# Kernel optimization log

Hardware: AMD Instinct MI355X
Metric: run time of the kernel (lower is better)

Reference implementation:

```python
import jax, jax.numpy as jnp
import numpy as np

N_NODES = 100000
N_EDGES = 1600000
F_IN = 128
F_OUT = 128


def setup_inputs() -> dict:
    key = jax.random.key(0)
    k1, k2, k3 = jax.random.split(key, 3)
    x = jax.random.normal(k1, (N_NODES, F_IN), dtype=jnp.float32)
    edge_index = jax.random.randint(k2, (2, N_EDGES), 0, N_NODES, dtype=jnp.int64)
    # glorot-ish init for GCNConv weight
    W = jax.random.normal(k3, (F_IN, F_OUT), dtype=jnp.float32) * (1.0 / np.sqrt(F_IN))
    b = jnp.zeros((F_OUT,), dtype=jnp.float32)
    return {"x": x, "edge_index": edge_index, "W": W, "b": b}


def gcn_conv(x, edge_index, W, b, num_nodes):
    # 1) linear transform
    h = x @ W  # [N, F_OUT]
    # 2) add self loops
    loop = jnp.arange(num_nodes, dtype=edge_index.dtype)
    src = jnp.concatenate([edge_index[0], loop])  # [E+N]
    dst = jnp.concatenate([edge_index[1], loop])  # [E+N]
    # 3) symmetric normalization: deg computed at targets (incl. self loops)
    ones = jnp.ones(src.shape[0], dtype=h.dtype)
    deg = jax.ops.segment_sum(ones, dst, num_segments=num_nodes)  # [N]
    dinv = jnp.where(deg > 0, jax.lax.rsqrt(deg), 0.0)
    norm = dinv[src] * dinv[dst]  # [E+N]
    # 4) message = norm * h[src]; scatter-add to dst
    msg = h[src] * norm[:, None]  # [E+N, F_OUT] (dominant memory traffic)
    out = jax.ops.segment_sum(msg, dst, num_segments=num_nodes)  # [N, F_OUT]
    return out + b


def reference(x, edge_index, W, b):
    out = gcn_conv(x, edge_index, W, b, N_NODES)
    return jax.nn.relu(out)
```

## Files before the change

### kernel.cpp

```cpp
#include <hip/hip_runtime.h>

#define F 128
#define CH 4096
#define BSH 9
#define BMSK ((1u << BSH) - 1u)

typedef __bf16 bf16x8 __attribute__((ext_vector_type(8)));
typedef float f32x4 __attribute__((ext_vector_type(4)));

__device__ inline uint32_t bfbits(float f) {
  uint32_t x = __float_as_uint(f);
  return (x + 0x7fffu + ((x >> 16) & 1u)) >> 16;
}
__device__ inline float blo(uint32_t u) { return __uint_as_float(u << 16); }
__device__ inline float bhi(uint32_t u) { return __uint_as_float(u & 0xffff0000u); }

__global__ __launch_bounds__(256) void k_gemm(const float* __restrict__ x,
                                              const float* __restrict__ W,
                                              const float* __restrict__ dinv,
                                              uint32_t* __restrict__ hB, int N) {
  __shared__ uint4 wb[2048];
  const int t = threadIdx.x;

#pragma unroll
  for (int p = 0; p < 8; ++p) {
    const int s = p * 256 + t;
    const int l = s & 63, nc = (s >> 6) & 7, kc = s >> 9;
    const int kbase = kc * 32 + ((l >> 4) << 3);
    const int col = nc * 16 + (l & 15);
    uint32_t q[4];
#pragma unroll
    for (int ii = 0; ii < 4; ++ii) {
      const uint32_t lo2 = bfbits(W[(size_t)(kbase + 2 * ii) * F + col]);
      const uint32_t hi2 = bfbits(W[(size_t)(kbase + 2 * ii + 1) * F + col]);
      q[ii] = lo2 | (hi2 << 16);
    }
    wb[s] = make_uint4(q[0], q[1], q[2], q[3]);
  }
  __syncthreads();

  const int w = t >> 6, l = t & 63;
  const int r0 = blockIdx.x * 64 + w * 16;
  const int arow = r0 + (l & 15);
  const int kb = (l >> 4) << 3;

  bf16x8 af[4];
#pragma unroll
  for (int kc = 0; kc < 4; ++kc) {
    float4 v0 = make_float4(0.f, 0.f, 0.f, 0.f), v1 = v0;
    if (arow < N) {
      v0 = *reinterpret_cast<const float4*>(&x[(size_t)arow * F + kc * 32 + kb]);
      v1 = *reinterpret_cast<const float4*>(&x[(size_t)arow * F + kc * 32 + kb + 4]);
    }
    const uint4 u = make_uint4(bfbits(v0.x) | (bfbits(v0.y) << 16),
                               bfbits(v0.z) | (bfbits(v0.w) << 16),
                               bfbits(v1.x) | (bfbits(v1.y) << 16),
                               bfbits(v1.z) | (bfbits(v1.w) << 16));
    af[kc] = __builtin_bit_cast(bf16x8, u);
  }

  f32x4 acc[8];
#pragma unroll
  for (int nc = 0; nc < 8; ++nc) acc[nc] = (f32x4){0.f, 0.f, 0.f, 0.f};

#pragma unroll
  for (int kc = 0; kc < 4; ++kc) {
#pragma unroll
    for (int nc = 0; nc < 8; ++nc) {
      const bf16x8 bf = __builtin_bit_cast(bf16x8, wb[(kc * 8 + nc) * 64 + l]);
      acc[nc] = __builtin_amdgcn_mfma_f32_16x16x32_bf16(af[kc], bf, acc[nc], 0, 0, 0);
    }
  }

  ushort* hBs = (ushort*)hB;
#pragma unroll
  for (int r = 0; r < 4; ++r) {
    const int row = r0 + ((l >> 4) << 2) + r;
    if (row < N) {
      const float dv = dinv[row];
#pragma unroll
      for (int nc = 0; nc < 8; ++nc)
        hBs[(size_t)row * F + nc * 16 + (l & 15)] = (ushort)bfbits(acc[nc][r] * dv);
    }
  }
}

__global__ __launch_bounds__(256) void k_hist(const int* __restrict__ dst,
                                              unsigned* __restrict__ bcnt, int E) {
  __shared__ unsigned h[256];
  const int t = threadIdx.x;
  h[t] = 0;
  __syncthreads();
  for (int i = blockIdx.x * 256 + t; i < E; i += gridDim.x * 256)
    atomicAdd(&h[(unsigned)dst[i] >> BSH], 1u);
  __syncthreads();
  if (h[t]) atomicAdd(&bcnt[t], h[t]);
}

__global__ __launch_bounds__(256) void k_scanB2(const unsigned* __restrict__ bcnt,
                                                unsigned* __restrict__ bstart,
                                                unsigned* __restrict__ bcur,
                                                int nbk, int E) {
  __shared__ unsigned sd[256];
  const int t = threadIdx.x;
  const unsigned v = (t < nbk) ? bcnt[t] : 0u;
  sd[t] = v;
  __syncthreads();
  for (int off = 1; off < 256; off <<= 1) {
    const unsigned u = (t >= off) ? sd[t - off] : 0u;
    __syncthreads();
    sd[t] += u;
    __syncthreads();
  }
  if (t < nbk) { const unsigned s = sd[t] - v; bstart[t] = s; bcur[t] = s; }
  if (t == 0) bstart[nbk] = (unsigned)E;
}

__global__ __launch_bounds__(256) void k_bucket(const int* __restrict__ src,
                                                const int* __restrict__ dst,
                                                unsigned* __restrict__ bcur,
                                                uint32_t* __restrict__ pairs,
                                                int E, int nbk) {
  __shared__ uint32_t sorted[CH];
  __shared__ unsigned hist[256], starts[256], cur[256], gb[256];
  const int t = threadIdx.x;
  const int c0 = blockIdx.x * CH;

  hist[t] = 0;
  __syncthreads();

  uint32_t pk[16];
  unsigned bk[16];
#pragma unroll
  for (int k = 0; k < 16; ++k) {
    const int i = c0 + k * 256 + t;
    if (i < E) {
      const unsigned s = (unsigned)src[i], d = (unsigned)dst[i];
      bk[k] = d >> BSH;
      pk[k] = (s << BSH) | (d & BMSK);
      atomicAdd(&hist[bk[k]], 1u);
    } else bk[k] = 0xffffffffu;
  }
  __syncthreads();

  cur[t] = hist[t];
  __syncthreads();
  for (int off = 1; off < 256; off <<= 1) {
    const unsigned u = (t >= off) ? cur[t - off] : 0u;
    __syncthreads();
    cur[t] += u;
    __syncthreads();
  }
  starts[t] = cur[t] - hist[t];
  __syncthreads();
  cur[t] = starts[t];
  if (t < nbk && hist[t] > 0) gb[t] = atomicAdd(&bcur[t], hist[t]);
  __syncthreads();

#pragma unroll
  for (int k = 0; k < 16; ++k) {
    if (bk[k] != 0xffffffffu) {
      const unsigned p = atomicAdd(&cur[bk[k]], 1u);
      sorted[p] = pk[k];
    }
  }
  __syncthreads();

  const int cnt = (c0 + CH <= E) ? CH : (E - c0);
  for (int idx = t; idx < cnt; idx += 256) {
    int lo = 0, hi = nbk - 1;
    while (lo < hi) {
      const int mid = (lo + hi + 1) >> 1;
      if ((int)starts[mid] <= idx) lo = mid; else hi = mid - 1;
    }
    pairs[gb[lo] + (idx - starts[lo])] = sorted[idx];
  }
}

__global__ __launch_bounds__(256) void k_pernode(const uint32_t* __restrict__ pairs,
                                                 const unsigned* __restrict__ bstart,
                                                 int* __restrict__ rowptr,
                                                 float* __restrict__ dinv,
                                                 int* __restrict__ esrc,
                                                 int N, int E) {
  __shared__ unsigned hist[512];
  __shared__ unsigned sd[256];
  const int b = blockIdx.x;
  const int t = threadIdx.x;
  const unsigned beg = bstart[b], end = bstart[b + 1];

  hist[t] = 0; hist[t + 256] = 0;
  __syncthreads();
  for (unsigned i = beg + t; i < end; i += 256)
    atomicAdd(&hist[pairs[i] & BMSK], 1u);
  __syncthreads();

  const unsigned d0 = hist[2 * t], d1 = hist[2 * t + 1];
  const unsigned tt = d0 + d1;
  sd[t] = tt;
  __syncthreads();
  for (int off = 1; off < 256; off <<= 1) {
    const unsigned u = (t >= off) ? sd[t - off] : 0u;
    __syncthreads();
    sd[t] += u;
    __syncthreads();
  }
  const unsigned base = sd[t] - tt;
  const unsigned r0 = base, r1 = base + d0;
  hist[2 * t] = r0; hist[2 * t + 1] = r1;

  const int node0 = b << BSH;
  const unsigned dd[2] = {d0, d1};
  const unsigned rr[2] = {r0, r1};
#pragma unroll
  for (int k = 0; k < 2; ++k) {
    const int node = node0 + 2 * t + k;
    if (node < N) {
      rowptr[node] = (int)(beg + rr[k]);
      dinv[node] = rsqrtf((float)dd[k] + 1.0f);
    }
  }
  if (b == 0 && t == 0) rowptr[N] = E;
  __syncthreads();

  for (unsigned i = beg + t; i < end; i += 256) {
    const uint32_t pk = pairs[i];
    const unsigned p = atomicAdd(&hist[pk & BMSK], 1u);
    esrc[beg + p] = (int)(pk >> BSH);
  }
}

__global__ __launch_bounds__(256) void k_gather(const uint32_t* __restrict__ hB,
                                                const float* __restrict__ dinv,
                                                const int* __restrict__ rowptr,
                                                const int* __restrict__ esrc,
                                                const float* __restrict__ bias,
                                                float* __restrict__ out, int N) {
  const int lane = threadIdx.x & 63;
  const int v = (int)((blockIdx.x * blockDim.x + threadIdx.x) >> 6);
  if (v >= N) return;
  const uint32_t* hL = hB + lane;
  const uint32_t u = hL[(size_t)v << 6];
  float a0 = blo(u), a1 = bhi(u);
  float b0 = 0.f, b1 = 0.f, c0 = 0.f, c1 = 0.f, e0 = 0.f, e1 = 0.f;
  const int beg = rowptr[v], end = rowptr[v + 1];
  for (int j0 = beg; j0 < end; j0 += 64) {
    const int cnt = min(64, end - j0);
    const int myS = (j0 + lane < end) ? esrc[j0 + lane] : 0;
    int k = 0;
    for (; k + 8 <= cnt; k += 8) {
      const int s0 = __shfl(myS, k),     s1 = __shfl(myS, k + 1);
      const int s2 = __shfl(myS, k + 2), s3 = __shfl(myS, k + 3);
      const int s4 = __shfl(myS, k + 4), s5 = __shfl(myS, k + 5);
      const int s6 = __shfl(myS, k + 6), s7 = __shfl(myS, k + 7);
      const uint32_t u0 = hL[(size_t)s0 << 6], u1 = hL[(size_t)s1 << 6];
      const uint32_t u2 = hL[(size_t)s2 << 6], u3 = hL[(size_t)s3 << 6];
      const uint32_t u4 = hL[(size_t)s4 << 6], u5 = hL[(size_t)s5 << 6];
      const uint32_t u6 = hL[(size_t)s6 << 6], u7 = hL[(size_t)s7 << 6];
      a0 += blo(u0); a1 += bhi(u0); b0 += blo(u1); b1 += bhi(u1);
      c0 += blo(u2); c1 += bhi(u2); e0 += blo(u3); e1 += bhi(u3);
      a0 += blo(u4); a1 += bhi(u4); b0 += blo(u5); b1 += bhi(u5);
      c0 += blo(u6); c1 += bhi(u6); e0 += blo(u7); e1 += bhi(u7);
    }
    for (; k < cnt; ++k) {
      const int s = __shfl(myS, k);
      const uint32_t us = hL[(size_t)s << 6];
      a0 += blo(us); a1 += bhi(us);
    }
  }
  a0 += b0 + c0 + e0;
  a1 += b1 + c1 + e1;
  const float dv = dinv[v];
  const int c = lane * 2;
  const float2 bv = *reinterpret_cast<const float2*>(&bias[c]);
  float2 r;
  r.x = fmaxf(fmaf(dv, a0, bv.x), 0.f);
  r.y = fmaxf(fmaf(dv, a1, bv.y), 0.f);
  *reinterpret_cast<float2*>(&out[(size_t)v * F + c]) = r;
}

extern "C" void kernel_launch(void* const* d_in, const int* in_sizes, int n_in,
                              void* d_out, int out_size, void* d_ws, size_t ws_size,
                              hipStream_t stream) {
  const float* x  = (const float*)d_in[0];
  const int*   ei = (const int*)d_in[1];
  const float* W  = (const float*)d_in[2];
  const float* b  = (const float*)d_in[3];
  float* out = (float*)d_out;

  const int N = in_sizes[0] / F;
  const int E = in_sizes[1] / 2;
  const int* srcA = ei;
  const int* dstA = ei + E;

  const int NB = (N + (1 << BSH) - 1) >> BSH;
  const int NCH = (E + CH - 1) / CH;

  auto aln = [](size_t v) { return (v + 255) & ~(size_t)255; };
  char* base = (char*)d_ws;
  size_t off = 0;
  uint32_t* hB = (uint32_t*)(base + off);     off += aln((size_t)N * (F / 2) * sizeof(uint32_t));
  int* esrc = (int*)(base + off);             off += aln((size_t)E * sizeof(int));
  uint32_t* pairs = (uint32_t*)(base + off);  off += aln((size_t)E * sizeof(uint32_t));
  float* dinv = (float*)(base + off);         off += aln((size_t)N * sizeof(float));
  int* rowptr = (int*)(base + off);           off += aln((size_t)(N + 1) * sizeof(int));
  unsigned* bcnt = (unsigned*)(base + off);   off += aln(256 * sizeof(unsigned));
  unsigned* bstart = (unsigned*)(base + off); off += aln(257 * sizeof(unsigned));
  unsigned* bcur = (unsigned*)(base + off);   off += aln(256 * sizeof(unsigned));

  hipMemsetAsync(bcnt, 0, 256 * sizeof(unsigned), stream);
  k_hist<<<256, 256, 0, stream>>>(dstA, bcnt, E);
  k_scanB2<<<1, 256, 0, stream>>>(bcnt, bstart, bcur, NB, E);
  k_bucket<<<NCH, 256, 0, stream>>>(srcA, dstA, bcur, pairs, E, NB);
  k_pernode<<<NB, 256, 0, stream>>>(pairs, bstart, rowptr, dinv, esrc, N, E);
  k_gemm<<<(N + 63) / 64, 256, 0, stream>>>(x, W, dinv, hB, N);
  k_gather<<<(N * 64 + 255) / 256, 256, 0, stream>>>(hB, dinv, rowptr, esrc, b, out, N);
}
```

Before: 242.5 us.

## Prepack W once, stage buckets in LDS, and split gather wave across two edges

```diff
diff --git a/kernel.cpp b/kernel.cpp
--- a/kernel.cpp
+++ b/kernel.cpp
@@ -4,6 +4,7 @@
 #define CH 4096
 #define BSH 9
 #define BMSK ((1u << BSH) - 1u)
+#define PCAP 9216
 
 typedef __bf16 bf16x8 __attribute__((ext_vector_type(8)));
 typedef float f32x4 __attribute__((ext_vector_type(4)));
@@ -15,28 +16,30 @@
 __device__ inline float blo(uint32_t u) { return __uint_as_float(u << 16); }
 __device__ inline float bhi(uint32_t u) { return __uint_as_float(u & 0xffff0000u); }
 
+__global__ __launch_bounds__(256) void k_prepW(const float* __restrict__ W,
+                                               uint4* __restrict__ wf) {
+  const int s = blockIdx.x * 256 + threadIdx.x;
+  const int l = s & 63, nc = (s >> 6) & 7, kc = s >> 9;
+  const int kbase = kc * 32 + ((l >> 4) << 3);
+  const int col = nc * 16 + (l & 15);
+  uint32_t q[4];
+#pragma unroll
+  for (int ii = 0; ii < 4; ++ii) {
+    const uint32_t lo2 = bfbits(W[(size_t)(kbase + 2 * ii) * F + col]);
+    const uint32_t hi2 = bfbits(W[(size_t)(kbase + 2 * ii + 1) * F + col]);
+    q[ii] = lo2 | (hi2 << 16);
+  }
+  wf[s] = make_uint4(q[0], q[1], q[2], q[3]);
+}
+
 __global__ __launch_bounds__(256) void k_gemm(const float* __restrict__ x,
-                                              const float* __restrict__ W,
+                                              const uint4* __restrict__ wf,
                                               const float* __restrict__ dinv,
                                               uint32_t* __restrict__ hB, int N) {
   __shared__ uint4 wb[2048];
   const int t = threadIdx.x;
-
-#pragma unroll
-  for (int p = 0; p < 8; ++p) {
-    const int s = p * 256 + t;
-    const int l = s & 63, nc = (s >> 6) & 7, kc = s >> 9;
-    const int kbase = kc * 32 + ((l >> 4) << 3);
-    const int col = nc * 16 + (l & 15);
-    uint32_t q[4];
-#pragma unroll
-    for (int ii = 0; ii < 4; ++ii) {
-      const uint32_t lo2 = bfbits(W[(size_t)(kbase + 2 * ii) * F + col]);
-      const uint32_t hi2 = bfbits(W[(size_t)(kbase + 2 * ii + 1) * F + col]);
-      q[ii] = lo2 | (hi2 << 16);
-    }
-    wb[s] = make_uint4(q[0], q[1], q[2], q[3]);
-  }
+#pragma unroll
+  for (int p = 0; p < 8; ++p) wb[p * 256 + t] = wf[p * 256 + t];
   __syncthreads();
 
   const int w = t >> 6, l = t & 63;
@@ -122,6 +125,7 @@
                                                 uint32_t* __restrict__ pairs,
                                                 int E, int nbk) {
   __shared__ uint32_t sorted[CH];
+  __shared__ unsigned char bkarr[CH];
   __shared__ unsigned hist[256], starts[256], cur[256], gb[256];
   const int t = threadIdx.x;
   const int c0 = blockIdx.x * CH;
@@ -162,17 +166,14 @@
     if (bk[k] != 0xffffffffu) {
       const unsigned p = atomicAdd(&cur[bk[k]], 1u);
       sorted[p] = pk[k];
+      bkarr[p] = (unsigned char)bk[k];
     }
   }
   __syncthreads();
 
   const int cnt = (c0 + CH <= E) ? CH : (E - c0);
   for (int idx = t; idx < cnt; idx += 256) {
-    int lo = 0, hi = nbk - 1;
-    while (lo < hi) {
-      const int mid = (lo + hi + 1) >> 1;
-      if ((int)starts[mid] <= idx) lo = mid; else hi = mid - 1;
-    }
+    const int lo = (int)bkarr[idx];
     pairs[gb[lo] + (idx - starts[lo])] = sorted[idx];
   }
 }
@@ -183,16 +184,22 @@
                                                  float* __restrict__ dinv,
                                                  int* __restrict__ esrc,
                                                  int N, int E) {
+  __shared__ uint32_t pl[PCAP];
   __shared__ unsigned hist[512];
   __shared__ unsigned sd[256];
   const int b = blockIdx.x;
   const int t = threadIdx.x;
   const unsigned beg = bstart[b], end = bstart[b + 1];
+  const int cnt = (int)(end - beg);
+  const bool inL = (cnt <= PCAP);
 
   hist[t] = 0; hist[t + 256] = 0;
-  __syncthreads();
-  for (unsigned i = beg + t; i < end; i += 256)
-    atomicAdd(&hist[pairs[i] & BMSK], 1u);
+  if (inL) for (int i = t; i < cnt; i += 256) pl[i] = pairs[beg + i];
+  __syncthreads();
+  for (int i = t; i < cnt; i += 256) {
+    const uint32_t pk = inL ? pl[i] : pairs[beg + i];
+    atomicAdd(&hist[pk & BMSK], 1u);
+  }
   __syncthreads();
 
   const unsigned d0 = hist[2 * t], d1 = hist[2 * t + 1];
@@ -223,8 +230,8 @@
   if (b == 0 && t == 0) rowptr[N] = E;
   __syncthreads();
 
-  for (unsigned i = beg + t; i < end; i += 256) {
-    const uint32_t pk = pairs[i];
+  for (int i = t; i < cnt; i += 256) {
+    const uint32_t pk = inL ? pl[i] : pairs[beg + i];
     const unsigned p = atomicAdd(&hist[pk & BMSK], 1u);
     esrc[beg + p] = (int)(pk >> BSH);
   }
@@ -236,47 +243,60 @@
                                                 const int* __restrict__ esrc,
                                                 const float* __restrict__ bias,
                                                 float* __restrict__ out, int N) {
-  const int lane = threadIdx.x & 63;
+  const int l = threadIdx.x & 63;
+  const int half = l >> 5;
+  const int lh = l & 31;
   const int v = (int)((blockIdx.x * blockDim.x + threadIdx.x) >> 6);
   if (v >= N) return;
-  const uint32_t* hL = hB + lane;
-  const uint32_t u = hL[(size_t)v << 6];
-  float a0 = blo(u), a1 = bhi(u);
-  float b0 = 0.f, b1 = 0.f, c0 = 0.f, c1 = 0.f, e0 = 0.f, e1 = 0.f;
+  const uint2* hR = reinterpret_cast<const uint2*>(hB) + lh;
+  float a0 = 0.f, a1 = 0.f, a2 = 0.f, a3 = 0.f;
+  float b0 = 0.f, b1 = 0.f, b2 = 0.f, b3 = 0.f;
   const int beg = rowptr[v], end = rowptr[v + 1];
   for (int j0 = beg; j0 < end; j0 += 64) {
     const int cnt = min(64, end - j0);
-    const int myS = (j0 + lane < end) ? esrc[j0 + lane] : 0;
+    const int myS = (j0 + l < end) ? esrc[j0 + l] : 0;
     int k = 0;
     for (; k + 8 <= cnt; k += 8) {
-      const int s0 = __shfl(myS, k),     s1 = __shfl(myS, k + 1);
-      const int s2 = __shfl(myS, k + 2), s3 = __shfl(myS, k + 3);
-      const int s4 = __shfl(myS, k + 4), s5 = __shfl(myS, k + 5);
-      const int s6 = __shfl(myS, k + 6), s7 = __shfl(myS, k + 7);
-      const uint32_t u0 = hL[(size_t)s0 << 6], u1 = hL[(size_t)s1 << 6];
-      const uint32_t u2 = hL[(size_t)s2 << 6], u3 = hL[(size_t)s3 << 6];
-      const uint32_t u4 = hL[(size_t)s4 << 6], u5 = hL[(size_t)s5 << 6];
-      const uint32_t u6 = hL[(size_t)s6 << 6], u7 = hL[(size_t)s7 << 6];
-      a0 += blo(u0); a1 += bhi(u0); b0 += blo(u1); b1 += bhi(u1);
-      c0 += blo(u2); c1 += bhi(u2); e0 += blo(u3); e1 += bhi(u3);
-      a0 += blo(u4); a1 += bhi(u4); b0 += blo(u5); b1 += bhi(u5);
-      c0 += blo(u6); c1 += bhi(u6); e0 += blo(u7); e1 += bhi(u7);
-    }
-    for (; k < cnt; ++k) {
-      const int s = __shfl(myS, k);
-      const uint32_t us = hL[(size_t)s << 6];
-      a0 += blo(us); a1 += bhi(us);
-    }
-  }
-  a0 += b0 + c0 + e0;
-  a1 += b1 + c1 + e1;
-  const float dv = dinv[v];
-  const int c = lane * 2;
-  const float2 bv = *reinterpret_cast<const float2*>(&bias[c]);
-  float2 r;
-  r.x = fmaxf(fmaf(dv, a0, bv.x), 0.f);
-  r.y = fmaxf(fmaf(dv, a1, bv.y), 0.f);
-  *reinterpret_cast<float2*>(&out[(size_t)v * F + c]) = r;
+      const int sE0 = __shfl(myS, k),     sO0 = __shfl(myS, k + 1);
+      const int sE1 = __shfl(myS, k + 2), sO1 = __shfl(myS, k + 3);
+      const int sE2 = __shfl(myS, k + 4), sO2 = __shfl(myS, k + 5);
+      const int sE3 = __shfl(myS, k + 6), sO3 = __shfl(myS, k + 7);
+      const uint2 u0 = hR[(size_t)(half ? sO0 : sE0) << 5];
+      const uint2 u1 = hR[(size_t)(half ? sO1 : sE1) << 5];
+      const uint2 u2 = hR[(size_t)(half ? sO2 : sE2) << 5];
+      const uint2 u3 = hR[(size_t)(half ? sO3 : sE3) << 5];
+      a0 += blo(u0.x); a1 += bhi(u0.x); a2 += blo(u0.y); a3 += bhi(u0.y);
+      b0 += blo(u1.x); b1 += bhi(u1.x); b2 += blo(u1.y); b3 += bhi(u1.y);
+      a0 += blo(u2.x); a1 += bhi(u2.x); a2 += blo(u2.y); a3 += bhi(u2.y);
+      b0 += blo(u3.x); b1 += bhi(u3.x); b2 += blo(u3.y); b3 += bhi(u3.y);
+    }
+    for (; k < cnt; k += 2) {
+      const int idx = k + half;
+      const int sE = __shfl(myS, k);
+      const int sO = __shfl(myS, min(k + 1, cnt - 1));
+      if (idx < cnt) {
+        const uint2 u = hR[(size_t)(half ? sO : sE) << 5];
+        a0 += blo(u.x); a1 += bhi(u.x); a2 += blo(u.y); a3 += bhi(u.y);
+      }
+    }
+  }
+  a0 += b0; a1 += b1; a2 += b2; a3 += b3;
+  a0 += __shfl_xor(a0, 32);
+  a1 += __shfl_xor(a1, 32);
+  a2 += __shfl_xor(a2, 32);
+  a3 += __shfl_xor(a3, 32);
+  if (half == 0) {
+    const uint2 us = hR[(size_t)v << 5];
+    a0 += blo(us.x); a1 += bhi(us.x); a2 += blo(us.y); a3 += bhi(us.y);
+    const float dv = dinv[v];
+    const float4 bv = *reinterpret_cast<const float4*>(&bias[lh * 4]);
+    float4 r;
+    r.x = fmaxf(fmaf(dv, a0, bv.x), 0.f);
+    r.y = fmaxf(fmaf(dv, a1, bv.y), 0.f);
+    r.z = fmaxf(fmaf(dv, a2, bv.z), 0.f);
+    r.w = fmaxf(fmaf(dv, a3, bv.w), 0.f);
+    *reinterpret_cast<float4*>(&out[(size_t)v * F + lh * 4]) = r;
+  }
 }
 
 extern "C" void kernel_launch(void* const* d_in, const int* in_sizes, int n_in,
@@ -307,12 +327,14 @@
   unsigned* bcnt = (unsigned*)(base + off);   off += aln(256 * sizeof(unsigned));
   unsigned* bstart = (unsigned*)(base + off); off += aln(257 * sizeof(unsigned));
   unsigned* bcur = (unsigned*)(base + off);   off += aln(256 * sizeof(unsigned));
+  uint4* wfrag = (uint4*)(base + off);        off += aln(2048 * sizeof(uint4));
 
   hipMemsetAsync(bcnt, 0, 256 * sizeof(unsigned), stream);
+  k_prepW<<<8, 256, 0, stream>>>(W, wfrag);
   k_hist<<<256, 256, 0, stream>>>(dstA, bcnt, E);
   k_scanB2<<<1, 256, 0, stream>>>(bcnt, bstart, bcur, NB, E);
   k_bucket<<<NCH, 256, 0, stream>>>(srcA, dstA, bcur, pairs, E, NB);
   k_pernode<<<NB, 256, 0, stream>>>(pairs, bstart, rowptr, dinv, esrc, N, E);
-  k_gemm<<<(N + 63) / 64, 256, 0, stream>>>(x, W, dinv, hB, N);
+  k_gemm<<<(N + 63) / 64, 256, 0, stream>>>(x, wfrag, dinv, hB, N);
   k_gather<<<(N * 64 + 255) / 256, 256, 0, stream>>>(hB, dinv, rowptr, esrc, b, out, N);
 }
```

Result: faster. 225.9 us (-6.9%).
